# Performance work log

Measured on AMD Instinct MI355X. Metric: run time of the kernel, lower is better.

The kernel has to match this reference:

```python
import jax, jax.numpy as jnp
import numpy as np

B, S, H, V, P = 16, 257, 768, 30522, 32  # batch, seq(incl CLS), hidden, vocab, tok_projection_dim


def setup_inputs() -> dict:
    key = jax.random.key(0)
    k1, k2, k3 = jax.random.split(key, 3)
    return {
        "hidden_states": jax.random.normal(k1, (B, S, H), jnp.float32),
        "logits": jax.random.normal(k2, (B, S, V), jnp.float32),
        "attention_mask": jnp.ones((B, S), jnp.float32),
        "W_tok": jax.random.normal(k3, (P, H), jnp.float32) * 0.02,
        "b_tok": jnp.zeros((P,), jnp.float32),
        "topk": 8,
    }


def reference(hidden_states, logits, attention_mask, W_tok, b_tok, topk):
    # strip [CLS] position, as in the torch forward
    hiddens = hidden_states[:, 1:, :]          # [B, S-1, H]
    mask = attention_mask[:, 1:]               # [B, S-1]
    lg = logits[:, 1:, :]                      # [B, S-1, V]

    full_router_repr = jnp.log1p(jax.nn.relu(lg)) * mask[:, :, None]   # [B, S-1, V]
    router_repr = jnp.max(full_router_repr, axis=1)                     # [B, V]

    expert_weights, expert_ids = jax.lax.top_k(full_router_repr, topk)  # [B, S-1, k]

    expert_repr = (jnp.einsum("bsh,ph->bsp", hiddens, W_tok) + b_tok) * mask[:, :, None]  # [B, S-1, P]

    b, s, v = full_router_repr.shape
    bi = jnp.arange(b)[:, None, None]
    si = jnp.arange(s)[None, :, None]
    router_mask = jnp.zeros_like(full_router_repr).at[bi, si, expert_ids].set(
        (expert_weights > 0.0).astype(full_router_repr.dtype)
    )                                                                   # [B, S-1, V]
    rm_seq = router_mask.sum(axis=1)                                    # [B, V]

    avg_cond_num_experts = rm_seq.sum(axis=1, keepdims=True).mean(axis=0, keepdims=True)  # [1, 1]
    avg_marg_num_experts = rm_seq.max(axis=0, keepdims=True).sum(axis=1, keepdims=True)   # [1, 1]

    router_softmax_sum = jax.nn.softmax(lg, axis=-1).sum(axis=1)        # [B, V]

    return (
        avg_cond_num_experts,
        avg_marg_num_experts,
        rm_seq,                # ret['router_mask']
        router_softmax_sum,    # ret['router_softmax_repr']
        mask,                  # ret['attention_mask']
        router_repr,
        expert_ids,
        expert_repr,
        expert_weights,
    )
```

## Files before the change

kernel.cpp:

```cpp
#include <hip/hip_runtime.h>
#include <hip/hip_bf16.h>
#include <float.h>

#define BB 16
#define SS 257
#define SP 256
#define HH 768
#define VV 30522
#define NF2 15261
#define PP 32
#define KK 8
#define CAP 2048

__global__ __launch_bounds__(256) void rowstats_kernel(
    const float* __restrict__ logits, const float* __restrict__ amask,
    float* __restrict__ invZ, float* __restrict__ o_rm,
    float* __restrict__ o_mask, float* __restrict__ o_ids,
    float* __restrict__ o_w)
{
  const int tid = threadIdx.x;
  const int row = blockIdx.x;
  const int b = row >> 8, s = row & 255;
  const float* lp = logits + (size_t)(b * SS + s + 1) * VV;
  const float mval = amask[b * SS + s + 1];
  const bool mz = (mval != 0.0f);

  __shared__ float cv[CAP];
  __shared__ int   ci[CAP];
  __shared__ float red[4];
  __shared__ int   cnt;
  if (tid == 0) cnt = 0;
  __syncthreads();

  const float2* lp2 = (const float2*)lp;
  const float T = 3.0f;
  float z0 = 0.0f, z1 = 0.0f, z2 = 0.0f, z3 = 0.0f;
  for (int k = 0; k < 56; k += 4) {
    float2 x0 = lp2[tid + 256 * (k + 0)];
    float2 x1 = lp2[tid + 256 * (k + 1)];
    float2 x2 = lp2[tid + 256 * (k + 2)];
    float2 x3 = lp2[tid + 256 * (k + 3)];
    z0 += __expf(x0.x) + __expf(x0.y);
    z1 += __expf(x1.x) + __expf(x1.y);
    z2 += __expf(x2.x) + __expf(x2.y);
    z3 += __expf(x3.x) + __expf(x3.y);
    if (mz) {
      if (x0.x > T) { int p = atomicAdd(&cnt, 1); if (p < CAP) { cv[p] = x0.x; ci[p] = 2 * (tid + 256 * (k + 0)); } }
      if (x0.y > T) { int p = atomicAdd(&cnt, 1); if (p < CAP) { cv[p] = x0.y; ci[p] = 2 * (tid + 256 * (k + 0)) + 1; } }
      if (x1.x > T) { int p = atomicAdd(&cnt, 1); if (p < CAP) { cv[p] = x1.x; ci[p] = 2 * (tid + 256 * (k + 1)); } }
      if (x1.y > T) { int p = atomicAdd(&cnt, 1); if (p < CAP) { cv[p] = x1.y; ci[p] = 2 * (tid + 256 * (k + 1)) + 1; } }
      if (x2.x > T) { int p = atomicAdd(&cnt, 1); if (p < CAP) { cv[p] = x2.x; ci[p] = 2 * (tid + 256 * (k + 2)); } }
      if (x2.y > T) { int p = atomicAdd(&cnt, 1); if (p < CAP) { cv[p] = x2.y; ci[p] = 2 * (tid + 256 * (k + 2)) + 1; } }
      if (x3.x > T) { int p = atomicAdd(&cnt, 1); if (p < CAP) { cv[p] = x3.x; ci[p] = 2 * (tid + 256 * (k + 3)); } }
      if (x3.y > T) { int p = atomicAdd(&cnt, 1); if (p < CAP) { cv[p] = x3.y; ci[p] = 2 * (tid + 256 * (k + 3)) + 1; } }
    }
  }
  for (int k = 56; k < 60; ++k) {
    int c = tid + 256 * k;
    if (c < NF2) {
      float2 x = lp2[c];
      z0 += __expf(x.x) + __expf(x.y);
      if (mz) {
        if (x.x > T) { int p = atomicAdd(&cnt, 1); if (p < CAP) { cv[p] = x.x; ci[p] = 2 * c; } }
        if (x.y > T) { int p = atomicAdd(&cnt, 1); if (p < CAP) { cv[p] = x.y; ci[p] = 2 * c + 1; } }
      }
    }
  }
  float zsum = (z0 + z1) + (z2 + z3);
  #pragma unroll
  for (int off = 32; off; off >>= 1) zsum += __shfl_xor(zsum, off, 64);
  if ((tid & 63) == 0) red[tid >> 6] = zsum;
  __syncthreads();
  if (tid == 0) invZ[row] = 1.0f / ((red[0] + red[1]) + (red[2] + red[3]));

  int n = cnt;
  if (n < KK || n > CAP) {
    float lv[KK]; int li[KK];
    #pragma unroll
    for (int j = 0; j < KK; ++j) { lv[j] = -1.0f; li[j] = 0; }
    for (int c = tid; c < NF2; c += 256) {
      float2 x = lp2[c];
      float v0 = mz ? fmaxf(x.x, 0.0f) : 0.0f;
      float v1 = mz ? fmaxf(x.y, 0.0f) : 0.0f;
      if (v0 > lv[KK - 1]) {
        #pragma unroll
        for (int j = KK - 1; j >= 1; --j) {
          bool a = lv[j - 1] < v0;
          bool q = lv[j] < v0;
          lv[j] = a ? lv[j - 1] : (q ? v0 : lv[j]);
          li[j] = a ? li[j - 1] : (q ? (2 * c) : li[j]);
        }
        if (lv[0] < v0) { lv[0] = v0; li[0] = 2 * c; }
      }
      if (v1 > lv[KK - 1]) {
        #pragma unroll
        for (int j = KK - 1; j >= 1; --j) {
          bool a = lv[j - 1] < v1;
          bool q = lv[j] < v1;
          lv[j] = a ? lv[j - 1] : (q ? v1 : lv[j]);
          li[j] = a ? li[j - 1] : (q ? (2 * c + 1) : li[j]);
        }
        if (lv[0] < v1) { lv[0] = v1; li[0] = 2 * c + 1; }
      }
    }
    #pragma unroll
    for (int j = 0; j < KK; ++j) { cv[tid * KK + j] = lv[j]; ci[tid * KK + j] = li[j]; }
    n = CAP;
    __syncthreads();
  }

  if (tid < 64) {
    #pragma unroll 1
    for (int kk = 0; kk < KK; ++kk) {
      float mv = -FLT_MAX; int mi = 0x7fffffff; int ms = -1;
      for (int j = tid; j < n; j += 64) {
        float v = cv[j]; int ix = ci[j];
        if (v > mv || (v == mv && ix < mi)) { mv = v; mi = ix; ms = j; }
      }
      #pragma unroll
      for (int off = 32; off; off >>= 1) {
        float ov = __shfl_xor(mv, off, 64);
        int   oi = __shfl_xor(mi, off, 64);
        int   os = __shfl_xor(ms, off, 64);
        if (ov > mv || (ov == mv && oi < mi)) { mv = ov; mi = oi; ms = os; }
      }
      if (tid == 0) cv[ms] = -FLT_MAX;
      if (tid == kk) {
        float w = mval * log1pf(fmaxf(mv, 0.0f));
        o_w[(size_t)row * KK + kk] = w;
        o_ids[(size_t)row * KK + kk] = (float)mi;
        if (w > 0.0f) atomicAdd(&o_rm[(size_t)b * VV + mi], 1.0f);
      }
    }
  }
  if (tid == 0) o_mask[row] = mval;
}

__global__ __launch_bounds__(256) void colstats_kernel(
    const float* __restrict__ logits, const float* __restrict__ amask,
    const float* __restrict__ invZ,
    float* __restrict__ o_rss, float* __restrict__ o_rrepr)
{
  const int b = blockIdx.y;
  const int tid = threadIdx.x;
  const int c = blockIdx.x * 256 + tid;
  __shared__ float zi[SP];
  __shared__ float mm[SP];
  zi[tid] = invZ[b * SP + tid];
  mm[tid] = amask[b * SS + 1 + tid];
  __syncthreads();
  if (c >= NF2) return;
  const float2* base = (const float2*)(logits + (size_t)(b * SS + 1) * VV) + c;
  float a0 = 0, a1 = 0, b0 = 0, b1 = 0, e0 = 0, e1 = 0, f0 = 0, f1 = 0;
  float g0 = 0, g1 = 0, h0 = 0, h1 = 0, i0 = 0, i1 = 0, j0 = 0, j1 = 0;
  #pragma unroll 2
  for (int s = 0; s < 64; ++s) {
    float2 x0 = base[(size_t)(s)       * NF2];
    float2 x1 = base[(size_t)(s +  64) * NF2];
    float2 x2 = base[(size_t)(s + 128) * NF2];
    float2 x3 = base[(size_t)(s + 192) * NF2];
    a0 = fmaf(__expf(x0.x), zi[s      ], a0);  a1 = fmaf(__expf(x0.y), zi[s      ], a1);
    b0 = fmaf(__expf(x1.x), zi[s +  64], b0);  b1 = fmaf(__expf(x1.y), zi[s +  64], b1);
    e0 = fmaf(__expf(x2.x), zi[s + 128], e0);  e1 = fmaf(__expf(x2.y), zi[s + 128], e1);
    f0 = fmaf(__expf(x3.x), zi[s + 192], f0);  f1 = fmaf(__expf(x3.y), zi[s + 192], f1);
    g0 = fmaxf(g0, mm[s      ] != 0.f ? x0.x : 0.f); g1 = fmaxf(g1, mm[s      ] != 0.f ? x0.y : 0.f);
    h0 = fmaxf(h0, mm[s +  64] != 0.f ? x1.x : 0.f); h1 = fmaxf(h1, mm[s +  64] != 0.f ? x1.y : 0.f);
    i0 = fmaxf(i0, mm[s + 128] != 0.f ? x2.x : 0.f); i1 = fmaxf(i1, mm[s + 128] != 0.f ? x2.y : 0.f);
    j0 = fmaxf(j0, mm[s + 192] != 0.f ? x3.x : 0.f); j1 = fmaxf(j1, mm[s + 192] != 0.f ? x3.y : 0.f);
  }
  float sa = (a0 + b0) + (e0 + f0);
  float sb = (a1 + b1) + (e1 + f1);
  float ma = fmaxf(fmaxf(g0, h0), fmaxf(i0, j0));
  float mb = fmaxf(fmaxf(g1, h1), fmaxf(i1, j1));
  size_t o = (size_t)b * VV + 2 * (size_t)c;
  *(float2*)(o_rss + o)   = make_float2(sa, sb);
  *(float2*)(o_rrepr + o) = make_float2(log1pf(ma), log1pf(mb));
}

__global__ __launch_bounds__(256) void transw_kernel(
    const float* __restrict__ W, float* __restrict__ Wt)
{
  int i = blockIdx.x * 256 + threadIdx.x;
  if (i < PP * HH) {
    int p = i / HH, k = i % HH;
    Wt[k * PP + p] = W[i];
  }
}

__global__ __launch_bounds__(256) void expertk_kernel(
    const float* __restrict__ hs, const float* __restrict__ amask,
    const float* __restrict__ Wt, const float* __restrict__ btok,
    float* __restrict__ o_er)
{
  const int row = blockIdx.x;
  const int b = row >> 8, s = row & 255;
  const float* hp = hs + (size_t)(b * SS + s + 1) * HH;
  __shared__ float h[HH];
  __shared__ float psum[8][PP];
  for (int i = threadIdx.x; i < HH; i += 256) h[i] = hp[i];
  __syncthreads();
  const int p = threadIdx.x & 31, g = threadIdx.x >> 5;
  float acc = 0.0f;
  #pragma unroll 8
  for (int k = g * 96; k < g * 96 + 96; ++k) acc = fmaf(h[k], Wt[k * PP + p], acc);
  psum[g][p] = acc;
  __syncthreads();
  if (threadIdx.x < PP) {
    float r = 0.0f;
    #pragma unroll
    for (int g2 = 0; g2 < 8; ++g2) r += psum[g2][threadIdx.x];
    float mval = amask[b * SS + s + 1];
    o_er[(size_t)row * PP + threadIdx.x] = (r + btok[threadIdx.x]) * mval;
  }
}

__global__ __launch_bounds__(256) void reducerm_kernel(
    const float* __restrict__ rm, float* __restrict__ out01)
{
  int v = blockIdx.x * 256 + threadIdx.x;
  float sm = 0.0f, mx = 0.0f;
  if (v < VV) {
    #pragma unroll
    for (int b = 0; b < BB; ++b) {
      float r = rm[(size_t)b * VV + v];
      sm += r; mx = fmaxf(mx, r);
    }
  }
  __shared__ float rs[256], rx[256];
  rs[threadIdx.x] = sm; rx[threadIdx.x] = mx;
  __syncthreads();
  #pragma unroll
  for (int st = 128; st > 0; st >>= 1) {
    if (threadIdx.x < st) {
      rs[threadIdx.x] += rs[threadIdx.x + st];
      rx[threadIdx.x] += rx[threadIdx.x + st];
    }
    __syncthreads();
  }
  if (threadIdx.x == 0) {
    atomicAdd(&out01[0], rs[0] * (1.0f / BB));
    atomicAdd(&out01[1], rx[0]);
  }
}

extern "C" void kernel_launch(void* const* d_in, const int* in_sizes, int n_in,
                              void* d_out, int out_size, void* d_ws, size_t ws_size,
                              hipStream_t stream) {
  const float* hs     = (const float*)d_in[0];
  const float* logits = (const float*)d_in[1];
  const float* amask  = (const float*)d_in[2];
  const float* W      = (const float*)d_in[3];
  const float* btok   = (const float*)d_in[4];

  float* out    = (float*)d_out;
  float* o_cond = out;
  float* o_rm   = out + 2;
  float* o_rss  = o_rm + (size_t)BB * VV;
  float* o_mask = o_rss + (size_t)BB * VV;
  float* o_rrepr= o_mask + (size_t)BB * SP;
  float* o_ids  = o_rrepr + (size_t)BB * VV;
  float* o_er   = o_ids + (size_t)BB * SP * KK;
  float* o_w    = o_er + (size_t)BB * SP * PP;

  float* wsf  = (float*)d_ws;
  float* invZ = wsf;
  float* Wt   = wsf + 4096;

  hipMemsetAsync(out, 0, (2 + (size_t)BB * VV) * sizeof(float), stream);

  rowstats_kernel<<<BB * SP, 256, 0, stream>>>(logits, amask, invZ, o_rm, o_mask, o_ids, o_w);
  colstats_kernel<<<dim3((NF2 + 255) / 256, BB), 256, 0, stream>>>(logits, amask, invZ, o_rss, o_rrepr);
  transw_kernel<<<(PP * HH + 255) / 256, 256, 0, stream>>>(W, Wt);
  expertk_kernel<<<BB * SP, 256, 0, stream>>>(hs, amask, Wt, btok, o_er);
  reducerm_kernel<<<(VV + 255) / 256, 256, 0, stream>>>(o_rm, o_cond);
}
```

Before: 785.7 us.

## Vectorize rowstats to float4 and fold small kernels into existing launches

The row-statistics pass now reads logits as aligned float4, using a per-row offset of 0 or 2 floats and a scalar tail handled by thread 0. It also adds a wave-wide __any pre-check so the candidate-collection atomics are skipped when no lane exceeds the threshold. The W transpose is folded into the first blocks of rowstats, and the router-mask reduction is folded into colstats. This removes two kernel launches and widens the memory loads, at the cost of more complex alignment handling and extra work in a few blocks.

```diff
diff --git a/kernel.cpp b/kernel.cpp
--- a/kernel.cpp
+++ b/kernel.cpp
@@ -8,22 +8,34 @@
 #define HH 768
 #define VV 30522
 #define NF2 15261
+#define NF4 7630
 #define PP 32
 #define KK 8
 #define CAP 2048
 
 __global__ __launch_bounds__(256) void rowstats_kernel(
     const float* __restrict__ logits, const float* __restrict__ amask,
+    const float* __restrict__ W, float* __restrict__ Wt,
     float* __restrict__ invZ, float* __restrict__ o_rm,
     float* __restrict__ o_mask, float* __restrict__ o_ids,
     float* __restrict__ o_w)
 {
   const int tid = threadIdx.x;
   const int row = blockIdx.x;
+
+  if (row < (PP * HH) / 256) {
+    int i = row * 256 + tid;
+    int p = i / HH, k = i - p * HH;
+    Wt[k * PP + p] = W[i];
+  }
+
   const int b = row >> 8, s = row & 255;
-  const float* lp = logits + (size_t)(b * SS + s + 1) * VV;
+  const int rg = b * SS + s + 1;
+  const float* lp = logits + (size_t)rg * VV;
   const float mval = amask[b * SS + s + 1];
   const bool mz = (mval != 0.0f);
+  const int ofs = (rg & 1) ? 2 : 0;
+  const float4* lp4 = (const float4*)(lp + ofs);
 
   __shared__ float cv[CAP];
   __shared__ int   ci[CAP];
@@ -32,40 +44,55 @@
   if (tid == 0) cnt = 0;
   __syncthreads();
 
-  const float2* lp2 = (const float2*)lp;
   const float T = 3.0f;
   float z0 = 0.0f, z1 = 0.0f, z2 = 0.0f, z3 = 0.0f;
-  for (int k = 0; k < 56; k += 4) {
-    float2 x0 = lp2[tid + 256 * (k + 0)];
-    float2 x1 = lp2[tid + 256 * (k + 1)];
-    float2 x2 = lp2[tid + 256 * (k + 2)];
-    float2 x3 = lp2[tid + 256 * (k + 3)];
-    z0 += __expf(x0.x) + __expf(x0.y);
-    z1 += __expf(x1.x) + __expf(x1.y);
-    z2 += __expf(x2.x) + __expf(x2.y);
-    z3 += __expf(x3.x) + __expf(x3.y);
-    if (mz) {
-      if (x0.x > T) { int p = atomicAdd(&cnt, 1); if (p < CAP) { cv[p] = x0.x; ci[p] = 2 * (tid + 256 * (k + 0)); } }
-      if (x0.y > T) { int p = atomicAdd(&cnt, 1); if (p < CAP) { cv[p] = x0.y; ci[p] = 2 * (tid + 256 * (k + 0)) + 1; } }
-      if (x1.x > T) { int p = atomicAdd(&cnt, 1); if (p < CAP) { cv[p] = x1.x; ci[p] = 2 * (tid + 256 * (k + 1)); } }
-      if (x1.y > T) { int p = atomicAdd(&cnt, 1); if (p < CAP) { cv[p] = x1.y; ci[p] = 2 * (tid + 256 * (k + 1)) + 1; } }
-      if (x2.x > T) { int p = atomicAdd(&cnt, 1); if (p < CAP) { cv[p] = x2.x; ci[p] = 2 * (tid + 256 * (k + 2)); } }
-      if (x2.y > T) { int p = atomicAdd(&cnt, 1); if (p < CAP) { cv[p] = x2.y; ci[p] = 2 * (tid + 256 * (k + 2)) + 1; } }
-      if (x3.x > T) { int p = atomicAdd(&cnt, 1); if (p < CAP) { cv[p] = x3.x; ci[p] = 2 * (tid + 256 * (k + 3)); } }
-      if (x3.y > T) { int p = atomicAdd(&cnt, 1); if (p < CAP) { cv[p] = x3.y; ci[p] = 2 * (tid + 256 * (k + 3)) + 1; } }
-    }
-  }
-  for (int k = 56; k < 60; ++k) {
-    int c = tid + 256 * k;
-    if (c < NF2) {
-      float2 x = lp2[c];
-      z0 += __expf(x.x) + __expf(x.y);
+
+  auto do4 = [&](float4 x, int fidx, float& za, float& zb) {
+    za += __expf(x.x) + __expf(x.y);
+    zb += __expf(x.z) + __expf(x.w);
+    float m4 = fmaxf(fmaxf(x.x, x.y), fmaxf(x.z, x.w));
+    if (__any(mz && (m4 > T))) {
       if (mz) {
-        if (x.x > T) { int p = atomicAdd(&cnt, 1); if (p < CAP) { cv[p] = x.x; ci[p] = 2 * c; } }
-        if (x.y > T) { int p = atomicAdd(&cnt, 1); if (p < CAP) { cv[p] = x.y; ci[p] = 2 * c + 1; } }
-      }
-    }
-  }
+        int v = ofs + 4 * fidx;
+        if (x.x > T) { int p = atomicAdd(&cnt, 1); if (p < CAP) { cv[p] = x.x; ci[p] = v;     } }
+        if (x.y > T) { int p = atomicAdd(&cnt, 1); if (p < CAP) { cv[p] = x.y; ci[p] = v + 1; } }
+        if (x.z > T) { int p = atomicAdd(&cnt, 1); if (p < CAP) { cv[p] = x.z; ci[p] = v + 2; } }
+        if (x.w > T) { int p = atomicAdd(&cnt, 1); if (p < CAP) { cv[p] = x.w; ci[p] = v + 3; } }
+      }
+    }
+  };
+
+  for (int k = 0; k < 28; k += 4) {
+    float4 x0 = lp4[tid + 256 * (k + 0)];
+    float4 x1 = lp4[tid + 256 * (k + 1)];
+    float4 x2 = lp4[tid + 256 * (k + 2)];
+    float4 x3 = lp4[tid + 256 * (k + 3)];
+    do4(x0, tid + 256 * (k + 0), z0, z1);
+    do4(x1, tid + 256 * (k + 1), z2, z3);
+    do4(x2, tid + 256 * (k + 2), z0, z1);
+    do4(x3, tid + 256 * (k + 3), z2, z3);
+  }
+  {
+    float4 x = lp4[tid + 256 * 28];
+    do4(x, tid + 256 * 28, z0, z1);
+  }
+  {
+    int f = tid + 256 * 29;
+    if (f < NF4) {
+      float4 x = lp4[f];
+      do4(x, f, z2, z3);
+    }
+  }
+  if (tid == 0) {
+    int l0 = ofs ? 0 : (NF4 * 4);
+    #pragma unroll
+    for (int j = 0; j < 2; ++j) {
+      float x = lp[l0 + j];
+      z0 += __expf(x);
+      if (mz && x > T) { int p = atomicAdd(&cnt, 1); if (p < CAP) { cv[p] = x; ci[p] = l0 + j; } }
+    }
+  }
+
   float zsum = (z0 + z1) + (z2 + z3);
   #pragma unroll
   for (int off = 32; off; off >>= 1) zsum += __shfl_xor(zsum, off, 64);
@@ -75,6 +102,7 @@
 
   int n = cnt;
   if (n < KK || n > CAP) {
+    const float2* lp2 = (const float2*)lp;
     float lv[KK]; int li[KK];
     #pragma unroll
     for (int j = 0; j < KK; ++j) { lv[j] = -1.0f; li[j] = 0; }
@@ -138,8 +166,9 @@
 
 __global__ __launch_bounds__(256) void colstats_kernel(
     const float* __restrict__ logits, const float* __restrict__ amask,
-    const float* __restrict__ invZ,
-    float* __restrict__ o_rss, float* __restrict__ o_rrepr)
+    const float* __restrict__ invZ, const float* __restrict__ rm,
+    float* __restrict__ o_rss, float* __restrict__ o_rrepr,
+    float* __restrict__ out01)
 {
   const int b = blockIdx.y;
   const int tid = threadIdx.x;
@@ -149,41 +178,60 @@
   zi[tid] = invZ[b * SP + tid];
   mm[tid] = amask[b * SS + 1 + tid];
   __syncthreads();
-  if (c >= NF2) return;
-  const float2* base = (const float2*)(logits + (size_t)(b * SS + 1) * VV) + c;
-  float a0 = 0, a1 = 0, b0 = 0, b1 = 0, e0 = 0, e1 = 0, f0 = 0, f1 = 0;
-  float g0 = 0, g1 = 0, h0 = 0, h1 = 0, i0 = 0, i1 = 0, j0 = 0, j1 = 0;
-  #pragma unroll 2
-  for (int s = 0; s < 64; ++s) {
-    float2 x0 = base[(size_t)(s)       * NF2];
-    float2 x1 = base[(size_t)(s +  64) * NF2];
-    float2 x2 = base[(size_t)(s + 128) * NF2];
-    float2 x3 = base[(size_t)(s + 192) * NF2];
-    a0 = fmaf(__expf(x0.x), zi[s      ], a0);  a1 = fmaf(__expf(x0.y), zi[s      ], a1);
-    b0 = fmaf(__expf(x1.x), zi[s +  64], b0);  b1 = fmaf(__expf(x1.y), zi[s +  64], b1);
-    e0 = fmaf(__expf(x2.x), zi[s + 128], e0);  e1 = fmaf(__expf(x2.y), zi[s + 128], e1);
-    f0 = fmaf(__expf(x3.x), zi[s + 192], f0);  f1 = fmaf(__expf(x3.y), zi[s + 192], f1);
-    g0 = fmaxf(g0, mm[s      ] != 0.f ? x0.x : 0.f); g1 = fmaxf(g1, mm[s      ] != 0.f ? x0.y : 0.f);
-    h0 = fmaxf(h0, mm[s +  64] != 0.f ? x1.x : 0.f); h1 = fmaxf(h1, mm[s +  64] != 0.f ? x1.y : 0.f);
-    i0 = fmaxf(i0, mm[s + 128] != 0.f ? x2.x : 0.f); i1 = fmaxf(i1, mm[s + 128] != 0.f ? x2.y : 0.f);
-    j0 = fmaxf(j0, mm[s + 192] != 0.f ? x3.x : 0.f); j1 = fmaxf(j1, mm[s + 192] != 0.f ? x3.y : 0.f);
-  }
-  float sa = (a0 + b0) + (e0 + f0);
-  float sb = (a1 + b1) + (e1 + f1);
-  float ma = fmaxf(fmaxf(g0, h0), fmaxf(i0, j0));
-  float mb = fmaxf(fmaxf(g1, h1), fmaxf(i1, j1));
-  size_t o = (size_t)b * VV + 2 * (size_t)c;
-  *(float2*)(o_rss + o)   = make_float2(sa, sb);
-  *(float2*)(o_rrepr + o) = make_float2(log1pf(ma), log1pf(mb));
-}
-
-__global__ __launch_bounds__(256) void transw_kernel(
-    const float* __restrict__ W, float* __restrict__ Wt)
-{
-  int i = blockIdx.x * 256 + threadIdx.x;
-  if (i < PP * HH) {
-    int p = i / HH, k = i % HH;
-    Wt[k * PP + p] = W[i];
+  if (c < NF2) {
+    const float2* base = (const float2*)(logits + (size_t)(b * SS + 1) * VV) + c;
+    float a0 = 0, a1 = 0, b0 = 0, b1 = 0, e0 = 0, e1 = 0, f0 = 0, f1 = 0;
+    float g0 = 0, g1 = 0, h0 = 0, h1 = 0, i0 = 0, i1 = 0, j0 = 0, j1 = 0;
+    #pragma unroll 2
+    for (int s = 0; s < 64; ++s) {
+      float2 x0 = base[(size_t)(s)       * NF2];
+      float2 x1 = base[(size_t)(s +  64) * NF2];
+      float2 x2 = base[(size_t)(s + 128) * NF2];
+      float2 x3 = base[(size_t)(s + 192) * NF2];
+      a0 = fmaf(__expf(x0.x), zi[s      ], a0);  a1 = fmaf(__expf(x0.y), zi[s      ], a1);
+      b0 = fmaf(__expf(x1.x), zi[s +  64], b0);  b1 = fmaf(__expf(x1.y), zi[s +  64], b1);
+      e0 = fmaf(__expf(x2.x), zi[s + 128], e0);  e1 = fmaf(__expf(x2.y), zi[s + 128], e1);
+      f0 = fmaf(__expf(x3.x), zi[s + 192], f0);  f1 = fmaf(__expf(x3.y), zi[s + 192], f1);
+      g0 = fmaxf(g0, mm[s      ] != 0.f ? x0.x : 0.f); g1 = fmaxf(g1, mm[s      ] != 0.f ? x0.y : 0.f);
+      h0 = fmaxf(h0, mm[s +  64] != 0.f ? x1.x : 0.f); h1 = fmaxf(h1, mm[s +  64] != 0.f ? x1.y : 0.f);
+      i0 = fmaxf(i0, mm[s + 128] != 0.f ? x2.x : 0.f); i1 = fmaxf(i1, mm[s + 128] != 0.f ? x2.y : 0.f);
+      j0 = fmaxf(j0, mm[s + 192] != 0.f ? x3.x : 0.f); j1 = fmaxf(j1, mm[s + 192] != 0.f ? x3.y : 0.f);
+    }
+    float sa = (a0 + b0) + (e0 + f0);
+    float sb = (a1 + b1) + (e1 + f1);
+    float ma = fmaxf(fmaxf(g0, h0), fmaxf(i0, j0));
+    float mb = fmaxf(fmaxf(g1, h1), fmaxf(i1, j1));
+    size_t o = (size_t)b * VV + 2 * (size_t)c;
+    *(float2*)(o_rss + o)   = make_float2(sa, sb);
+    *(float2*)(o_rrepr + o) = make_float2(log1pf(ma), log1pf(mb));
+  }
+
+  const int fb = blockIdx.y * gridDim.x + blockIdx.x;
+  if (fb < (VV + 255) / 256) {
+    int v = fb * 256 + tid;
+    float sm = 0.0f, mx = 0.0f;
+    if (v < VV) {
+      #pragma unroll
+      for (int b2 = 0; b2 < BB; ++b2) {
+        float r = rm[(size_t)b2 * VV + v];
+        sm += r; mx = fmaxf(mx, r);
+      }
+    }
+    __shared__ float rs[256], rx[256];
+    rs[tid] = sm; rx[tid] = mx;
+    __syncthreads();
+    #pragma unroll
+    for (int st = 128; st > 0; st >>= 1) {
+      if (tid < st) {
+        rs[tid] += rs[tid + st];
+        rx[tid] += rx[tid + st];
+      }
+      __syncthreads();
+    }
+    if (tid == 0) {
+      atomicAdd(&out01[0], rs[0] * (1.0f / BB));
+      atomicAdd(&out01[1], rx[0]);
+    }
   }
 }
 
@@ -214,35 +262,6 @@
   }
 }
 
-__global__ __launch_bounds__(256) void reducerm_kernel(
-    const float* __restrict__ rm, float* __restrict__ out01)
-{
-  int v = blockIdx.x * 256 + threadIdx.x;
-  float sm = 0.0f, mx = 0.0f;
-  if (v < VV) {
-    #pragma unroll
-    for (int b = 0; b < BB; ++b) {
-      float r = rm[(size_t)b * VV + v];
-      sm += r; mx = fmaxf(mx, r);
-    }
-  }
-  __shared__ float rs[256], rx[256];
-  rs[threadIdx.x] = sm; rx[threadIdx.x] = mx;
-  __syncthreads();
-  #pragma unroll
-  for (int st = 128; st > 0; st >>= 1) {
-    if (threadIdx.x < st) {
-      rs[threadIdx.x] += rs[threadIdx.x + st];
-      rx[threadIdx.x] += rx[threadIdx.x + st];
-    }
-    __syncthreads();
-  }
-  if (threadIdx.x == 0) {
-    atomicAdd(&out01[0], rs[0] * (1.0f / BB));
-    atomicAdd(&out01[1], rx[0]);
-  }
-}
-
 extern "C" void kernel_launch(void* const* d_in, const int* in_sizes, int n_in,
                               void* d_out, int out_size, void* d_ws, size_t ws_size,
                               hipStream_t stream) {
@@ -268,9 +287,7 @@
 
   hipMemsetAsync(out, 0, (2 + (size_t)BB * VV) * sizeof(float), stream);
 
-  rowstats_kernel<<<BB * SP, 256, 0, stream>>>(logits, amask, invZ, o_rm, o_mask, o_ids, o_w);
-  colstats_kernel<<<dim3((NF2 + 255) / 256, BB), 256, 0, stream>>>(logits, amask, invZ, o_rss, o_rrepr);
-  transw_kernel<<<(PP * HH + 255) / 256, 256, 0, stream>>>(W, Wt);
+  rowstats_kernel<<<BB * SP, 256, 0, stream>>>(logits, amask, W, Wt, invZ, o_rm, o_mask, o_ids, o_w);
+  colstats_kernel<<<dim3((NF2 + 255) / 256, BB), 256, 0, stream>>>(logits, amask, invZ, o_rm, o_rss, o_rrepr, o_cond);
   expertk_kernel<<<BB * SP, 256, 0, stream>>>(hs, amask, Wt, btok, o_er);
-  reducerm_kernel<<<(VV + 255) / 256, 256, 0, stream>>>(o_rm, o_cond);
-}
+}
```

After: 778.0 us. About the same (-1.0%).
